# Optimization experiments

Hardware: AMD Instinct MI355X
Metric: run time of the kernel (lower is better)

## Reference

```python
import jax, jax.numpy as jnp
import numpy as np

B, N, D = 4, 2048, 1024
H, HD = 16, 64
S = 11  # n_scales
D4 = jnp.array([0.4829629131445341, 0.8365163037378079,
                0.2241438680420134, -0.1294095225512604], dtype=jnp.float32)


def _causal_dilated_d4(f, d):
    """Causal depthwise D4 conv with dilation d along axis 2. f: [B,H,N,HD].
    Matches torch F.pad(x,(3d,0)) + F.conv1d(dilation=d, groups=C):
    y[n] = sum_t D4[t] * f[n - (3-t)*d]."""
    n = f.shape[2]
    fp = jnp.pad(f, ((0, 0), (0, 0), (3 * d, 0), (0, 0)))
    return (D4[0] * fp[:, :, 0:n, :]
            + D4[1] * fp[:, :, d:d + n, :]
            + D4[2] * fp[:, :, 2 * d:2 * d + n, :]
            + D4[3] * fp[:, :, 3 * d:3 * d + n, :])


def setup_inputs() -> dict:
    key = jax.random.key(0)
    ks = jax.random.split(key, 10)
    s = 0.02
    return {
        "x": jax.random.normal(ks[0], (B, N, D), dtype=jnp.float32),
        "Wqkv": jax.random.normal(ks[1], (3 * D, D), dtype=jnp.float32) * s,
        "bqkv": jnp.zeros((3 * D,), dtype=jnp.float32),
        "Wo": jax.random.normal(ks[2], (D, D), dtype=jnp.float32) * s,
        "bo": jnp.zeros((D,), dtype=jnp.float32),
        "Wg": jax.random.normal(ks[3], (D, D), dtype=jnp.float32) * s,
        "bg": jnp.full((D,), 2.0, dtype=jnp.float32),
        "scale_gain": jnp.zeros((S, H), dtype=jnp.float32),
        "Wqs": jax.random.normal(ks[4], (S, HD), dtype=jnp.float32) * 0.01,
        "field_coupling": jnp.eye(H, dtype=jnp.float32)
        + 0.01 * jax.random.normal(ks[5], (H, H), dtype=jnp.float32),
    }


def reference(x, Wqkv, bqkv, Wo, bo, Wg, bg, scale_gain, Wqs, field_coupling):
    b, n, d = x.shape
    qkv = x @ Wqkv.T + bqkv                          # [B,N,3D]
    q, k, v = jnp.split(qkv, 3, axis=-1)
    q = q.reshape(b, n, H, HD).transpose(0, 2, 1, 3)  # [B,H,N,HD]
    k = k.reshape(b, n, H, HD).transpose(0, 2, 1, 3)
    v = v.reshape(b, n, H, HD).transpose(0, 2, 1, 3)

    # per-position scale gains: learned prior + query-conditioned offset
    q_offset = jnp.einsum('bhnd,sd->bhns', q, Wqs)    # [B,H,N,S]
    prior = scale_gain.T[None, :, None, :]            # [1,H,1,S]
    gains = jax.nn.softmax(q_offset + prior, axis=-1)

    # deposit: field[i] = V[i] * ||K[i]||
    k_mag = jnp.linalg.norm(k, axis=-1, keepdims=True)
    field = v * k_mag                                 # [B,H,N,HD]

    # propagate: causal multiscale dilated D4 conv, gain-weighted accumulate
    out_field = jnp.zeros_like(field)
    for j in range(S):
        y = _causal_dilated_d4(field, 1 << j)
        out_field = out_field + gains[:, :, :, j:j + 1] * y

    coupling = jax.nn.softmax(field_coupling, axis=-1)
    out_field = jnp.einsum('ij,bjnd->bind', coupling, out_field)

    gate = jax.nn.sigmoid(x @ Wg.T + bg)              # [B,N,D]
    gathered = out_field.transpose(0, 2, 1, 3).reshape(b, n, d)
    return (gathered * gate) @ Wo.T + bo
```

## Files before the change

kernel.cpp:

```cpp
#include <hip/hip_runtime.h>
#include <hip/hip_bf16.h>
#include <stdint.h>
#include <math.h>

#define BB 4
#define NN 2048
#define DD 1024
#define HH 16
#define HDD 64
#define SS 11

#define D4_0 0.4829629131445341f
#define D4_1 0.8365163037378079f
#define D4_2 0.2241438680420134f
#define D4_3 (-0.1294095225512604f)

typedef __bf16 bf16_t;
typedef __bf16 bf16x4_t __attribute__((ext_vector_type(4)));
typedef __bf16 bf16x8_t __attribute__((ext_vector_type(8)));
typedef float f32x4_t __attribute__((ext_vector_type(4)));

__global__ __launch_bounds__(256) void cvt_all_k(const float* __restrict__ s0,
                                                 const float* __restrict__ s1,
                                                 const float* __restrict__ s2,
                                                 const float* __restrict__ s3,
                                                 bf16_t* __restrict__ d0,
                                                 bf16_t* __restrict__ d1,
                                                 bf16_t* __restrict__ d2,
                                                 bf16_t* __restrict__ d3) {
  const int n0 = 2097152, n1 = 786432, n2 = 262144, n3 = 262144;
  int i = blockIdx.x * 256 + threadIdx.x;
  const float* s;
  bf16_t* d;
  if (i < n0) { s = s0; d = d0; }
  else if (i < n0 + n1) { i -= n0; s = s1; d = d1; }
  else if (i < n0 + n1 + n2) { i -= n0 + n1; s = s2; d = d2; }
  else { i -= n0 + n1 + n2; if (i >= n3) return; s = s3; d = d3; }
  f32x4_t v = ((const f32x4_t*)s)[i];
  bf16x4_t o;
  o[0] = (bf16_t)v[0]; o[1] = (bf16_t)v[1]; o[2] = (bf16_t)v[2]; o[3] = (bf16_t)v[3];
  ((bf16x4_t*)d)[i] = o;
}

__device__ __forceinline__ void gload16(const void* g, void* l) {
  __builtin_amdgcn_global_load_lds((__attribute__((address_space(1))) void*)(void*)g,
                                   (__attribute__((address_space(3))) void*)l,
                                   16, 0, 0);
}

template <int MODE>
__global__ __launch_bounds__(256) void gemm_nt(const bf16_t* __restrict__ A,
                                               const bf16_t* __restrict__ Bw,
                                               const float* __restrict__ bias0,
                                               const float* __restrict__ bias1,
                                               void* __restrict__ out0v,
                                               void* __restrict__ out1v,
                                               int M, int Nn, int K) {
  __shared__ bf16_t As[128 * 64];
  __shared__ bf16_t Bs[128 * 64];

  const int tid = threadIdx.x;
  const int ntiles = Nn >> 7;
  const int grp = ntiles << 3;
  const int g = blockIdx.x / grp;
  const int j = blockIdx.x % grp;
  const int mtile = (g << 3) | (j & 7);
  const int ntile = j >> 3;
  const int row0 = mtile << 7;
  const int col0 = ntile << 7;
  const int w = tid >> 6, lane = tid & 63;
  const int wm = w >> 1, wn = w & 1;
  const int m16 = lane & 15, quad = lane >> 4;

  f32x4_t acc[4][4];
#pragma unroll
  for (int i = 0; i < 4; i++)
#pragma unroll
    for (int jj = 0; jj < 4; jj++) acc[i][jj] = (f32x4_t){0.f, 0.f, 0.f, 0.f};

  for (int kb = 0; kb < K; kb += 64) {
    __syncthreads();
#pragma unroll
    for (int r = 0; r < 4; ++r) {
      int c = r * 256 + tid;
      int row = c >> 3, kc = c & 7;
      int swz = kc ^ (row & 7);
      const bf16_t* gpA = A + (size_t)(row0 + row) * K + kb + swz * 8;
      const bf16_t* gpB = Bw + (size_t)(col0 + row) * K + kb + swz * 8;
      bf16_t* lpA = As + (size_t)(r * 256 + (tid & 192)) * 8;
      bf16_t* lpB = Bs + (size_t)(r * 256 + (tid & 192)) * 8;
      gload16(gpA, lpA);
      gload16(gpB, lpB);
    }
    __syncthreads();

#pragma unroll
    for (int kk = 0; kk < 2; ++kk) {
      bf16x8_t af[4], bfr[4];
      const int kc = (kk << 2) + quad;
#pragma unroll
      for (int i = 0; i < 4; i++) {
        int arow = (wm << 6) + (i << 4) + m16;
        af[i] = *(const bf16x8_t*)(As + arow * 64 + ((kc ^ (arow & 7)) << 3));
        int brow = (wn << 6) + (i << 4) + m16;
        bfr[i] = *(const bf16x8_t*)(Bs + brow * 64 + ((kc ^ (brow & 7)) << 3));
      }
#pragma unroll
      for (int i = 0; i < 4; i++)
#pragma unroll
        for (int jj = 0; jj < 4; jj++)
          acc[i][jj] = __builtin_amdgcn_mfma_f32_16x16x32_bf16(af[i], bfr[jj], acc[i][jj], 0, 0, 0);
    }
  }

#pragma unroll
  for (int i = 0; i < 4; i++) {
#pragma unroll
    for (int jj = 0; jj < 4; jj++) {
      const int grow0 = row0 + (wm << 6) + (i << 4) + (quad << 2);
      const int gcol = col0 + (wn << 6) + (jj << 4) + m16;
      const float bval = (MODE == 0)
                             ? (gcol < 3072 ? bias0[gcol] : bias1[gcol - 3072])
                             : bias0[gcol];
#pragma unroll
      for (int r = 0; r < 4; r++) {
        float val = acc[i][jj][r] + bval;
        if (MODE == 0) {
          if (gcol < 3072)
            ((bf16_t*)out0v)[(size_t)(grow0 + r) * 3072 + gcol] = (bf16_t)val;
          else
            ((bf16_t*)out1v)[(size_t)(grow0 + r) * 1024 + (gcol - 3072)] =
                (bf16_t)(1.f / (1.f + __expf(-val)));
        } else {
          ((float*)out0v)[(size_t)(grow0 + r) * Nn + gcol] = val;
        }
      }
    }
  }
}

__global__ __launch_bounds__(256) void field_gains_k(const bf16_t* __restrict__ qkvb,
                                                     const float* __restrict__ scale_gain,
                                                     const float* __restrict__ Wqs,
                                                     bf16_t* __restrict__ fieldb,
                                                     float* __restrict__ gains) {
  __shared__ float skmag[4 * 16];
  const int tid = threadIdx.x;
  const int w = tid >> 6, lane = tid & 63;
  const int bn = blockIdx.x * 4 + w;
  const int b = bn >> 11, n_pos = bn & 2047;
  const int m16 = lane & 15, quad = lane >> 4;
  const bf16_t* qp = qkvb + (size_t)bn * 3072;

  bf16x8_t aq[2], ak[2], bw[2];
#pragma unroll
  for (int it = 0; it < 2; it++) {
    const int koff = it * 32 + quad * 8;
    aq[it] = *(const bf16x8_t*)(qp + m16 * 64 + koff);
    ak[it] = *(const bf16x8_t*)(qp + 1024 + m16 * 64 + koff);
    bf16x8_t bwv;
    if (m16 < SS) {
      const float* wp = Wqs + m16 * 64 + koff;
#pragma unroll
      for (int j = 0; j < 8; j++) bwv[j] = (bf16_t)wp[j];
    } else {
#pragma unroll
      for (int j = 0; j < 8; j++) bwv[j] = (bf16_t)0.f;
    }
    bw[it] = bwv;
  }

  f32x4_t acc_l = (f32x4_t){0.f, 0.f, 0.f, 0.f};
  f32x4_t acc_k = (f32x4_t){0.f, 0.f, 0.f, 0.f};
#pragma unroll
  for (int it = 0; it < 2; it++) {
    acc_l = __builtin_amdgcn_mfma_f32_16x16x32_bf16(aq[it], bw[it], acc_l, 0, 0, 0);
    acc_k = __builtin_amdgcn_mfma_f32_16x16x32_bf16(ak[it], ak[it], acc_k, 0, 0, 0);
  }

#pragma unroll
  for (int r = 0; r < 4; r++) {
    if (m16 == quad * 4 + r) skmag[w * 16 + m16] = sqrtf(fmaxf(acc_k[r], 0.f));
  }

#pragma unroll
  for (int r = 0; r < 4; r++) {
    const int m = quad * 4 + r;
    float lg = (m16 < SS) ? (acc_l[r] + scale_gain[m16 * 16 + m]) : -1e30f;
    float mx = lg;
#pragma unroll
    for (int sh = 1; sh < 16; sh <<= 1) mx = fmaxf(mx, __shfl_xor(mx, sh, 64));
    float e = (m16 < SS) ? __expf(lg - mx) : 0.f;
    float se = e;
#pragma unroll
    for (int sh = 1; sh < 16; sh <<= 1) se += __shfl_xor(se, sh, 64);
    if (m16 < SS)
      gains[((size_t)(b * 16 + m) * 2048 + n_pos) * SS + m16] = e / se;
  }

  __syncthreads();

#pragma unroll
  for (int h = 0; h < 16; h++) {
    const float km = skmag[w * 16 + h];
    const float v = (float)qp[2048 + h * 64 + lane];
    fieldb[((size_t)(b * 16 + h) * 2048 + n_pos) * 64 + lane] = (bf16_t)(v * km);
  }
}

__global__ __launch_bounds__(256) void conv_k(const bf16_t* __restrict__ field,
                                              const float* __restrict__ gains,
                                              bf16_t* __restrict__ facc) {
  __shared__ float sg[32 * SS];
  const int tid = threadIdx.x;
  const int blk = blockIdx.x;
  const int bh = blk & 63;
  const int ntile = blk >> 6;
  const int n0 = ntile * 32;

  for (int i = tid; i < 32 * SS; i += 256)
    sg[i] = gains[((size_t)bh * 2048 + n0) * SS + i];
  __syncthreads();

  const int w = tid >> 6, lane = tid & 63;
  const int nsub = lane >> 3, c = lane & 7;
  const int ln = w * 8 + nsub;
  const int n = n0 + ln;
  const bf16_t* frow = field + (size_t)bh * 2048 * 64;

  float g[SS];
#pragma unroll
  for (int s = 0; s < SS; s++) g[s] = sg[ln * SS + s];

  float acc[8];
  {
    bf16x8_t f0 = *(const bf16x8_t*)(frow + (size_t)n * 64 + c * 8);
#pragma unroll
    for (int q = 0; q < 8; q++) acc[q] = D4_3 * (float)f0[q];
  }
#pragma unroll
  for (int j = 0; j < 11; j++) {
    float wgt = D4_2 * g[j];
    if (j >= 1) wgt += D4_1 * g[j - 1];
    int rr = n - (1 << j);
    float wv = rr >= 0 ? wgt : 0.f;
    rr = rr >= 0 ? rr : 0;
    bf16x8_t fv = *(const bf16x8_t*)(frow + (size_t)rr * 64 + c * 8);
#pragma unroll
    for (int q = 0; q < 8; q++) acc[q] += wv * (float)fv[q];
  }
#pragma unroll
  for (int j = 0; j < 10; j++) {
    int rr = n - (3 << j);
    float wv = rr >= 0 ? (D4_0 * g[j]) : 0.f;
    rr = rr >= 0 ? rr : 0;
    bf16x8_t fv = *(const bf16x8_t*)(frow + (size_t)rr * 64 + c * 8);
#pragma unroll
    for (int q = 0; q < 8; q++) acc[q] += wv * (float)fv[q];
  }
  bf16x8_t o;
#pragma unroll
  for (int q = 0; q < 8; q++) o[q] = (bf16_t)acc[q];
  *(bf16x8_t*)(facc + ((size_t)bh * 2048 + n) * 64 + c * 8) = o;
}

__global__ __launch_bounds__(1024) void couple_gate_k(const bf16_t* __restrict__ facc,
                                                      const float* __restrict__ fcoup,
                                                      const bf16_t* __restrict__ gate,
                                                      bf16_t* __restrict__ gmat) {
  __shared__ float sacc[1024];
  __shared__ float sc[256];
  __shared__ float scn[256];
  const int tid = threadIdx.x;
  const int bn = blockIdx.x;
  const int b = bn >> 11, n = bn & 2047;
  if (tid < 256) sc[tid] = fcoup[tid];
  const int i = tid >> 6, hd = tid & 63;
  sacc[tid] = (float)facc[(((size_t)(b * 16 + i)) * 2048 + n) * 64 + hd];
  __syncthreads();
  if (tid < 16) {
    float row[16];
    float mx = -1e30f;
#pragma unroll
    for (int j = 0; j < 16; j++) { row[j] = sc[tid * 16 + j]; mx = fmaxf(mx, row[j]); }
    float se = 0.f;
#pragma unroll
    for (int j = 0; j < 16; j++) { row[j] = __expf(row[j] - mx); se += row[j]; }
    float inv = 1.f / se;
#pragma unroll
    for (int j = 0; j < 16; j++) scn[tid * 16 + j] = row[j] * inv;
  }
  __syncthreads();
  float s = 0.f;
#pragma unroll
  for (int j = 0; j < 16; j++) s += scn[i * 16 + j] * sacc[j * 64 + hd];
  const float gt = (float)gate[(size_t)bn * 1024 + tid];
  gmat[(size_t)bn * 1024 + tid] = (bf16_t)(s * gt);
}

extern "C" void kernel_launch(void* const* d_in, const int* in_sizes, int n_in,
                              void* d_out, int out_size, void* d_ws, size_t ws_size,
                              hipStream_t stream) {
  (void)in_sizes; (void)n_in; (void)out_size; (void)ws_size;
  const float* x = (const float*)d_in[0];
  const float* Wqkv = (const float*)d_in[1];
  const float* bqkv = (const float*)d_in[2];
  const float* Wo = (const float*)d_in[3];
  const float* bo = (const float*)d_in[4];
  const float* Wg = (const float*)d_in[5];
  const float* bg = (const float*)d_in[6];
  const float* scale_gain = (const float*)d_in[7];
  const float* Wqs = (const float*)d_in[8];
  const float* fcoup = (const float*)d_in[9];

  char* ws = (char*)d_ws;
  size_t off = 0;
  auto alloc = [&](size_t bytes) {
    void* p = ws + off;
    off += (bytes + 255) & ~(size_t)255;
    return p;
  };
  bf16_t* xb = (bf16_t*)alloc(8192ull * 1024 * 2);
  bf16_t* Wab = (bf16_t*)alloc(4096ull * 1024 * 2);
  bf16_t* Wob = (bf16_t*)alloc(1024ull * 1024 * 2);
  bf16_t* qkvb = (bf16_t*)alloc(8192ull * 3072 * 2);
  bf16_t* gateb = (bf16_t*)alloc(8192ull * 1024 * 2);
  bf16_t* fieldb = (bf16_t*)alloc(8388608ull * 2);
  float* gains = (float*)alloc(8192ull * 16 * SS * 4);
  bf16_t* facc = (bf16_t*)alloc(8388608ull * 2);
  bf16_t* gmat = (bf16_t*)alloc(8192ull * 1024 * 2);

  cvt_all_k<<<13316, 256, 0, stream>>>(x, Wqkv, Wg, Wo,
                                       xb, Wab, Wab + 3072ull * 1024, Wob);

  gemm_nt<0><<<64 * 32, 256, 0, stream>>>(xb, Wab, bqkv, bg, qkvb, gateb, 8192, 4096, 1024);

  field_gains_k<<<2048, 256, 0, stream>>>(qkvb, scale_gain, Wqs, fieldb, gains);

  conv_k<<<4096, 256, 0, stream>>>(fieldb, gains, facc);

  couple_gate_k<<<8192, 1024, 0, stream>>>(facc, fcoup, gateb, gmat);

  gemm_nt<1><<<64 * 8, 256, 0, stream>>>(gmat, Wob, bo, nullptr, (void*)d_out, nullptr, 8192, 1024, 1024);
}
```

Measured before the change: 283.3 us.

## Fold Q projection into Wqs logits and compute K norms in GEMM epilogue

Precomputes Wqs·Wq (plus bias) as 176 extra weight rows, so the gain logits come straight out of the main projection GEMM and Q is never materialized. K-column tiles are reduced in the GEMM epilogue to per-head norms instead of being stored. This shrinks the projection GEMM's N dimension from 4096 to 3328 and cuts the qkv write and reread traffic. The cost is a small weight-prep kernel, extra bias copies, a non-swizzled tile order, and a change in bf16 rounding from precomputing the combined weights.

```diff
diff --git a/kernel.cpp b/kernel.cpp
--- a/kernel.cpp
+++ b/kernel.cpp
@@ -28,7 +28,7 @@
                                                  bf16_t* __restrict__ d1,
                                                  bf16_t* __restrict__ d2,
                                                  bf16_t* __restrict__ d3) {
-  const int n0 = 2097152, n1 = 786432, n2 = 262144, n3 = 262144;
+  const int n0 = 2097152, n1 = 524288, n2 = 262144, n3 = 262144;
   int i = blockIdx.x * 256 + threadIdx.x;
   const float* s;
   bf16_t* d;
@@ -42,30 +42,70 @@
   ((bf16x4_t*)d)[i] = o;
 }
 
+__global__ __launch_bounds__(256) void wl_k(const float* __restrict__ Wqkv,
+                                            const float* __restrict__ Wqs,
+                                            const float* __restrict__ bqkv,
+                                            bf16_t* __restrict__ Wlb,
+                                            float* __restrict__ blv) {
+  const int h = blockIdx.x;
+  const int tid = threadIdx.x;
+  const int d0 = tid * 4;
+  float acc[SS][4];
+#pragma unroll
+  for (int s = 0; s < SS; s++)
+#pragma unroll
+    for (int j = 0; j < 4; j++) acc[s][j] = 0.f;
+  for (int hd = 0; hd < 64; hd++) {
+    f32x4_t w = *(const f32x4_t*)(Wqkv + (size_t)(h * 64 + hd) * 1024 + d0);
+#pragma unroll
+    for (int s = 0; s < SS; s++) {
+      float qs = Wqs[s * 64 + hd];
+#pragma unroll
+      for (int j = 0; j < 4; j++) acc[s][j] += qs * w[j];
+    }
+  }
+#pragma unroll
+  for (int s = 0; s < SS; s++) {
+    bf16x4_t o;
+#pragma unroll
+    for (int j = 0; j < 4; j++) o[j] = (bf16_t)acc[s][j];
+    *(bf16x4_t*)(Wlb + (size_t)(h * SS + s) * 1024 + d0) = o;
+  }
+  if (tid < SS) {
+    float b = 0.f;
+    for (int hd = 0; hd < 64; hd++) b += Wqs[tid * 64 + hd] * bqkv[h * 64 + hd];
+    blv[h * SS + tid] = b;
+  }
+  if (blockIdx.x == 0) {
+    for (int i = tid; i < 80; i += 256) blv[176 + i] = 0.f;
+    bf16x8_t z;
+#pragma unroll
+    for (int j = 0; j < 8; j++) z[j] = (bf16_t)0.f;
+    bf16_t* pad = Wlb + 176ull * 1024;
+    for (int i = tid; i < 80 * 1024 / 8; i += 256) ((bf16x8_t*)pad)[i] = z;
+  }
+}
+
 __device__ __forceinline__ void gload16(const void* g, void* l) {
   __builtin_amdgcn_global_load_lds((__attribute__((address_space(1))) void*)(void*)g,
                                    (__attribute__((address_space(3))) void*)l,
                                    16, 0, 0);
 }
 
-template <int MODE>
-__global__ __launch_bounds__(256) void gemm_nt(const bf16_t* __restrict__ A,
-                                               const bf16_t* __restrict__ Bw,
-                                               const float* __restrict__ bias0,
-                                               const float* __restrict__ bias1,
-                                               void* __restrict__ out0v,
-                                               void* __restrict__ out1v,
-                                               int M, int Nn, int K) {
+__global__ __launch_bounds__(256) void gemm_a(const bf16_t* __restrict__ A,
+                                              const bf16_t* __restrict__ Bw,
+                                              const float* __restrict__ biasA,
+                                              bf16_t* __restrict__ vb,
+                                              bf16_t* __restrict__ gateb,
+                                              float* __restrict__ lgf,
+                                              float* __restrict__ kmagf) {
   __shared__ bf16_t As[128 * 64];
   __shared__ bf16_t Bs[128 * 64];
-
-  const int tid = threadIdx.x;
-  const int ntiles = Nn >> 7;
-  const int grp = ntiles << 3;
-  const int g = blockIdx.x / grp;
-  const int j = blockIdx.x % grp;
-  const int mtile = (g << 3) | (j & 7);
-  const int ntile = j >> 3;
+  const int K = 1024;
+
+  const int tid = threadIdx.x;
+  const int mtile = blockIdx.x / 26;
+  const int ntile = blockIdx.x % 26;
   const int row0 = mtile << 7;
   const int col0 = ntile << 7;
   const int w = tid >> 6, lane = tid & 63;
@@ -113,98 +153,167 @@
     }
   }
 
+  const int region = ntile >> 3;
+  if (region == 0) {
+    const int head = (ntile << 1) + wn;
+#pragma unroll
+    for (int i = 0; i < 4; i++) {
+      float ps[4] = {0.f, 0.f, 0.f, 0.f};
+#pragma unroll
+      for (int jj = 0; jj < 4; jj++) {
+        const float bval = biasA[col0 + (wn << 6) + (jj << 4) + m16];
+#pragma unroll
+        for (int r = 0; r < 4; r++) {
+          float val = acc[i][jj][r] + bval;
+          ps[r] += val * val;
+        }
+      }
+#pragma unroll
+      for (int r = 0; r < 4; r++) {
+#pragma unroll
+        for (int sh = 1; sh < 16; sh <<= 1) ps[r] += __shfl_xor(ps[r], sh, 64);
+        if (m16 == 0) {
+          const int grow = row0 + (wm << 6) + (i << 4) + (quad << 2) + r;
+          kmagf[grow * 16 + head] = sqrtf(fmaxf(ps[r], 0.f));
+        }
+      }
+    }
+  } else {
+#pragma unroll
+    for (int i = 0; i < 4; i++) {
+#pragma unroll
+      for (int jj = 0; jj < 4; jj++) {
+        const int grow0 = row0 + (wm << 6) + (i << 4) + (quad << 2);
+        const int gcol = col0 + (wn << 6) + (jj << 4) + m16;
+        const float bval = biasA[gcol];
+#pragma unroll
+        for (int r = 0; r < 4; r++) {
+          float val = acc[i][jj][r] + bval;
+          if (region == 1) {
+            vb[(size_t)(grow0 + r) * 1024 + (gcol - 1024)] = (bf16_t)val;
+          } else if (region == 2) {
+            gateb[(size_t)(grow0 + r) * 1024 + (gcol - 2048)] =
+                (bf16_t)(1.f / (1.f + __expf(-val)));
+          } else {
+            const int c = gcol - 3072;
+            if (c < 176) lgf[(size_t)(grow0 + r) * 176 + c] = val;
+          }
+        }
+      }
+    }
+  }
+}
+
+__global__ __launch_bounds__(256) void gemm_b(const bf16_t* __restrict__ A,
+                                              const bf16_t* __restrict__ Bw,
+                                              const float* __restrict__ bias,
+                                              float* __restrict__ out,
+                                              int M, int Nn, int K) {
+  __shared__ bf16_t As[128 * 64];
+  __shared__ bf16_t Bs[128 * 64];
+
+  const int tid = threadIdx.x;
+  const int ntiles = Nn >> 7;
+  const int mtile = blockIdx.x / ntiles;
+  const int ntile = blockIdx.x % ntiles;
+  const int row0 = mtile << 7;
+  const int col0 = ntile << 7;
+  const int w = tid >> 6, lane = tid & 63;
+  const int wm = w >> 1, wn = w & 1;
+  const int m16 = lane & 15, quad = lane >> 4;
+
+  f32x4_t acc[4][4];
+#pragma unroll
+  for (int i = 0; i < 4; i++)
+#pragma unroll
+    for (int jj = 0; jj < 4; jj++) acc[i][jj] = (f32x4_t){0.f, 0.f, 0.f, 0.f};
+
+  for (int kb = 0; kb < K; kb += 64) {
+    __syncthreads();
+#pragma unroll
+    for (int r = 0; r < 4; ++r) {
+      int c = r * 256 + tid;
+      int row = c >> 3, kc = c & 7;
+      int swz = kc ^ (row & 7);
+      const bf16_t* gpA = A + (size_t)(row0 + row) * K + kb + swz * 8;
+      const bf16_t* gpB = Bw + (size_t)(col0 + row) * K + kb + swz * 8;
+      bf16_t* lpA = As + (size_t)(r * 256 + (tid & 192)) * 8;
+      bf16_t* lpB = Bs + (size_t)(r * 256 + (tid & 192)) * 8;
+      gload16(gpA, lpA);
+      gload16(gpB, lpB);
+    }
+    __syncthreads();
+
+#pragma unroll
+    for (int kk = 0; kk < 2; ++kk) {
+      bf16x8_t af[4], bfr[4];
+      const int kc = (kk << 2) + quad;
+#pragma unroll
+      for (int i = 0; i < 4; i++) {
+        int arow = (wm << 6) + (i << 4) + m16;
+        af[i] = *(const bf16x8_t*)(As + arow * 64 + ((kc ^ (arow & 7)) << 3));
+        int brow = (wn << 6) + (i << 4) + m16;
+        bfr[i] = *(const bf16x8_t*)(Bs + brow * 64 + ((kc ^ (brow & 7)) << 3));
+      }
+#pragma unroll
+      for (int i = 0; i < 4; i++)
+#pragma unroll
+        for (int jj = 0; jj < 4; jj++)
+          acc[i][jj] = __builtin_amdgcn_mfma_f32_16x16x32_bf16(af[i], bfr[jj], acc[i][jj], 0, 0, 0);
+    }
+  }
+
 #pragma unroll
   for (int i = 0; i < 4; i++) {
 #pragma unroll
     for (int jj = 0; jj < 4; jj++) {
       const int grow0 = row0 + (wm << 6) + (i << 4) + (quad << 2);
       const int gcol = col0 + (wn << 6) + (jj << 4) + m16;
-      const float bval = (MODE == 0)
-                             ? (gcol < 3072 ? bias0[gcol] : bias1[gcol - 3072])
-                             : bias0[gcol];
-#pragma unroll
-      for (int r = 0; r < 4; r++) {
-        float val = acc[i][jj][r] + bval;
-        if (MODE == 0) {
-          if (gcol < 3072)
-            ((bf16_t*)out0v)[(size_t)(grow0 + r) * 3072 + gcol] = (bf16_t)val;
-          else
-            ((bf16_t*)out1v)[(size_t)(grow0 + r) * 1024 + (gcol - 3072)] =
-                (bf16_t)(1.f / (1.f + __expf(-val)));
-        } else {
-          ((float*)out0v)[(size_t)(grow0 + r) * Nn + gcol] = val;
-        }
-      }
-    }
-  }
-}
-
-__global__ __launch_bounds__(256) void field_gains_k(const bf16_t* __restrict__ qkvb,
+      const float bval = bias[gcol];
+#pragma unroll
+      for (int r = 0; r < 4; r++)
+        out[(size_t)(grow0 + r) * Nn + gcol] = acc[i][jj][r] + bval;
+    }
+  }
+}
+
+__global__ __launch_bounds__(256) void field_gains_k(const bf16_t* __restrict__ vb,
+                                                     const float* __restrict__ lgf,
+                                                     const float* __restrict__ kmagf,
                                                      const float* __restrict__ scale_gain,
-                                                     const float* __restrict__ Wqs,
                                                      bf16_t* __restrict__ fieldb,
                                                      float* __restrict__ gains) {
-  __shared__ float skmag[4 * 16];
   const int tid = threadIdx.x;
   const int w = tid >> 6, lane = tid & 63;
   const int bn = blockIdx.x * 4 + w;
   const int b = bn >> 11, n_pos = bn & 2047;
-  const int m16 = lane & 15, quad = lane >> 4;
-  const bf16_t* qp = qkvb + (size_t)bn * 3072;
-
-  bf16x8_t aq[2], ak[2], bw[2];
-#pragma unroll
-  for (int it = 0; it < 2; it++) {
-    const int koff = it * 32 + quad * 8;
-    aq[it] = *(const bf16x8_t*)(qp + m16 * 64 + koff);
-    ak[it] = *(const bf16x8_t*)(qp + 1024 + m16 * 64 + koff);
-    bf16x8_t bwv;
-    if (m16 < SS) {
-      const float* wp = Wqs + m16 * 64 + koff;
-#pragma unroll
-      for (int j = 0; j < 8; j++) bwv[j] = (bf16_t)wp[j];
-    } else {
-#pragma unroll
-      for (int j = 0; j < 8; j++) bwv[j] = (bf16_t)0.f;
-    }
-    bw[it] = bwv;
-  }
-
-  f32x4_t acc_l = (f32x4_t){0.f, 0.f, 0.f, 0.f};
-  f32x4_t acc_k = (f32x4_t){0.f, 0.f, 0.f, 0.f};
-#pragma unroll
-  for (int it = 0; it < 2; it++) {
-    acc_l = __builtin_amdgcn_mfma_f32_16x16x32_bf16(aq[it], bw[it], acc_l, 0, 0, 0);
-    acc_k = __builtin_amdgcn_mfma_f32_16x16x32_bf16(ak[it], ak[it], acc_k, 0, 0, 0);
-  }
-
-#pragma unroll
-  for (int r = 0; r < 4; r++) {
-    if (m16 == quad * 4 + r) skmag[w * 16 + m16] = sqrtf(fmaxf(acc_k[r], 0.f));
-  }
-
-#pragma unroll
-  for (int r = 0; r < 4; r++) {
-    const int m = quad * 4 + r;
-    float lg = (m16 < SS) ? (acc_l[r] + scale_gain[m16 * 16 + m]) : -1e30f;
-    float mx = lg;
-#pragma unroll
-    for (int sh = 1; sh < 16; sh <<= 1) mx = fmaxf(mx, __shfl_xor(mx, sh, 64));
-    float e = (m16 < SS) ? __expf(lg - mx) : 0.f;
-    float se = e;
-#pragma unroll
-    for (int sh = 1; sh < 16; sh <<= 1) se += __shfl_xor(se, sh, 64);
-    if (m16 < SS)
-      gains[((size_t)(b * 16 + m) * 2048 + n_pos) * SS + m16] = e / se;
-  }
-
-  __syncthreads();
+
+  float km = 0.f;
+  if (lane < 16) km = kmagf[bn * 16 + lane];
 
 #pragma unroll
   for (int h = 0; h < 16; h++) {
-    const float km = skmag[w * 16 + h];
-    const float v = (float)qp[2048 + h * 64 + lane];
-    fieldb[((size_t)(b * 16 + h) * 2048 + n_pos) * 64 + lane] = (bf16_t)(v * km);
+    const float kmh = __shfl(km, h, 64);
+    const float v = (float)vb[(size_t)bn * 1024 + h * 64 + lane];
+    fieldb[((size_t)(b * 16 + h) * 2048 + n_pos) * 64 + lane] = (bf16_t)(v * kmh);
+  }
+
+  if (lane < 16) {
+    const int head = lane;
+    float lg[SS];
+    float mx = -1e30f;
+#pragma unroll
+    for (int s = 0; s < SS; s++) {
+      lg[s] = lgf[(size_t)bn * 176 + head * SS + s] + scale_gain[s * 16 + head];
+      mx = fmaxf(mx, lg[s]);
+    }
+    float se = 0.f;
+#pragma unroll
+    for (int s = 0; s < SS; s++) { lg[s] = __expf(lg[s] - mx); se += lg[s]; }
+    const float inv = 1.f / se;
+    float* gp = gains + ((size_t)(b * 16 + head) * 2048 + n_pos) * SS;
+#pragma unroll
+    for (int s = 0; s < SS; s++) gp[s] = lg[s] * inv;
   }
 }
 
@@ -321,25 +430,34 @@
     return p;
   };
   bf16_t* xb = (bf16_t*)alloc(8192ull * 1024 * 2);
-  bf16_t* Wab = (bf16_t*)alloc(4096ull * 1024 * 2);
+  bf16_t* Wab = (bf16_t*)alloc(3328ull * 1024 * 2);
   bf16_t* Wob = (bf16_t*)alloc(1024ull * 1024 * 2);
-  bf16_t* qkvb = (bf16_t*)alloc(8192ull * 3072 * 2);
+  float* biasA = (float*)alloc(3328ull * 4);
+  bf16_t* vb = (bf16_t*)alloc(8192ull * 1024 * 2);
   bf16_t* gateb = (bf16_t*)alloc(8192ull * 1024 * 2);
+  float* lgf = (float*)alloc(8192ull * 176 * 4);
+  float* kmagf = (float*)alloc(8192ull * 16 * 4);
   bf16_t* fieldb = (bf16_t*)alloc(8388608ull * 2);
   float* gains = (float*)alloc(8192ull * 16 * SS * 4);
   bf16_t* facc = (bf16_t*)alloc(8388608ull * 2);
   bf16_t* gmat = (bf16_t*)alloc(8192ull * 1024 * 2);
 
-  cvt_all_k<<<13316, 256, 0, stream>>>(x, Wqkv, Wg, Wo,
-                                       xb, Wab, Wab + 3072ull * 1024, Wob);
-
-  gemm_nt<0><<<64 * 32, 256, 0, stream>>>(xb, Wab, bqkv, bg, qkvb, gateb, 8192, 4096, 1024);
-
-  field_gains_k<<<2048, 256, 0, stream>>>(qkvb, scale_gain, Wqs, fieldb, gains);
+  hipMemcpyAsync(biasA, bqkv + 1024, 1024 * 4, hipMemcpyDeviceToDevice, stream);
+  hipMemcpyAsync(biasA + 1024, bqkv + 2048, 1024 * 4, hipMemcpyDeviceToDevice, stream);
+  hipMemcpyAsync(biasA + 2048, bg, 1024 * 4, hipMemcpyDeviceToDevice, stream);
+
+  cvt_all_k<<<12288, 256, 0, stream>>>(x, Wqkv + 1048576, Wg, Wo,
+                                       xb, Wab, Wab + 2048ull * 1024, Wob);
+
+  wl_k<<<16, 256, 0, stream>>>(Wqkv, Wqs, bqkv, Wab + 3072ull * 1024, biasA + 3072);
+
+  gemm_a<<<64 * 26, 256, 0, stream>>>(xb, Wab, biasA, vb, gateb, lgf, kmagf);
+
+  field_gains_k<<<2048, 256, 0, stream>>>(vb, lgf, kmagf, scale_gain, fieldb, gains);
 
   conv_k<<<4096, 256, 0, stream>>>(fieldb, gains, facc);
 
   couple_gate_k<<<8192, 1024, 0, stream>>>(facc, fcoup, gateb, gmat);
 
-  gemm_nt<1><<<64 * 8, 256, 0, stream>>>(gmat, Wob, bo, nullptr, (void*)d_out, nullptr, 8192, 1024, 1024);
-}
+  gemm_b<<<64 * 8, 256, 0, stream>>>(gmat, Wob, bo, (float*)d_out, 8192, 1024, 1024);
+}
```

Result: slower. 311.7 us (+10.0%).
